# Kernel optimization log

Hardware: AMD Instinct MI355X
Metric: run time of the kernel (lower is better)

The kernel has to match this reference:

```python
import jax, jax.numpy as jnp
import numpy as np
import math

B, S, H = 2, 2048, 2048
NH, NKV, HD = 16, 8, 128          # heads, kv heads, head_dim
GROUPS = NH // NKV                 # 2
FF = 5632
EPS = 1e-6
SCALE = 0.02


def setup_inputs() -> dict:
    key = jax.random.key(0)
    ks = jax.random.split(key, 12)
    def w(k, shape):
        return jax.random.normal(k, shape, dtype=jnp.float32) * SCALE
    # additive causal mask: 0 on/below diagonal, -inf above
    causal = jnp.where(jnp.tril(jnp.ones((S, S), dtype=bool)), 0.0, -jnp.inf)
    attention_mask = causal[None, None].astype(jnp.float32)  # [1,1,S,S]
    return {
        "hidden_states": jax.random.normal(ks[0], (B, S, H), dtype=jnp.float32),
        "attention_mask": attention_mask,
        "q_w": w(ks[1], (NH * HD, H)),      # nn.Linear convention [out, in]
        "k_w": w(ks[2], (NKV * HD, H)),
        "v_w": w(ks[3], (NKV * HD, H)),
        "o_w": w(ks[4], (H, NH * HD)),
        "gate_w": w(ks[5], (FF, H)),
        "up_w": w(ks[6], (FF, H)),
        "down_w": w(ks[7], (H, FF)),
        "ln1_w": jnp.ones((H,), dtype=jnp.float32),
        "ln2_w": jnp.ones((H,), dtype=jnp.float32),
    }


def rmsnorm(x, w):
    var = jnp.mean(jnp.square(x), axis=-1, keepdims=True)
    return x * jax.lax.rsqrt(var + EPS) * w


def attention(x, mask, q_w, k_w, v_w, o_w):
    b, s, _ = x.shape
    q = (x @ q_w.T).reshape(b, s, NH, HD).transpose(0, 2, 1, 3)    # [b,nh,s,hd]
    k = (x @ k_w.T).reshape(b, s, NKV, HD).transpose(0, 2, 1, 3)   # [b,nkv,s,hd]
    v = (x @ v_w.T).reshape(b, s, NKV, HD).transpose(0, 2, 1, 3)
    # GQA: repeat_interleave kv heads to match query heads
    k = jnp.repeat(k, GROUPS, axis=1)
    v = jnp.repeat(v, GROUPS, axis=1)
    scores = jnp.einsum("bhqd,bhkd->bhqk", q, k) / math.sqrt(HD) + mask
    probs = jax.nn.softmax(scores.astype(jnp.float32), axis=-1).astype(q.dtype)
    out = jnp.einsum("bhqk,bhkd->bhqd", probs, v)
    out = out.transpose(0, 2, 1, 3).reshape(b, s, NH * HD)
    return out @ o_w.T


def mlp(x, gate_w, up_w, down_w):
    return (jax.nn.silu(x @ gate_w.T) * (x @ up_w.T)) @ down_w.T


def reference(hidden_states, attention_mask, q_w, k_w, v_w, o_w,
              gate_w, up_w, down_w, ln1_w, ln2_w):
    # pre-norm transformer layer with residuals
    h = hidden_states + attention(rmsnorm(hidden_states, ln1_w), attention_mask,
                                  q_w, k_w, v_w, o_w)
    out = h + mlp(rmsnorm(h, ln2_w), gate_w, up_w, down_w)
    return out
```

## Files before the change

kernel.cpp:

```cpp
#include <hip/hip_runtime.h>
#include <stdint.h>

typedef __bf16 bf16_t;
typedef __bf16 bf16x8 __attribute__((ext_vector_type(8)));
typedef __bf16 bf16x4 __attribute__((ext_vector_type(4)));
typedef float  f32x4  __attribute__((ext_vector_type(4)));

#define MFMA16(a, b, c) __builtin_amdgcn_mfma_f32_16x16x32_bf16((a), (b), (c), 0, 0, 0)

__device__ __forceinline__ void load_lds16(const bf16_t* g, bf16_t* l)
{
    __builtin_amdgcn_global_load_lds(
        (const __attribute__((address_space(1))) uint32_t*)(uintptr_t)g,
        (__attribute__((address_space(3))) uint32_t*)(uint32_t)(uintptr_t)l,
        16, 0, 0);
}

__device__ __forceinline__ void lds_stage2(const bf16_t* __restrict__ Gsrc,
                                           bf16_t* Ldst, int u0,
                                           int tid, int K, int k0)
{
#pragma unroll
    for (int l = 0; l < 2; ++l) {
        int u = u0 + l * 512 + tid;
        int row = u >> 3;
        int col = (((u & 7) ^ (row & 7)) << 3);
        load_lds16(Gsrc + (size_t)row * K + k0 + col, Ldst + u * 8);
    }
}

__global__ __launch_bounds__(256)
void wconv(const float* __restrict__ X, bf16_t* __restrict__ Y, int n)
{
    int i = (blockIdx.x * 256 + threadIdx.x) * 8;
    if (i >= n) return;
    f32x4 a = *(const f32x4*)(X + i);
    f32x4 b = *(const f32x4*)(X + i + 4);
    bf16x8 y;
#pragma unroll
    for (int e = 0; e < 4; ++e) { y[e] = (bf16_t)a[e]; y[e + 4] = (bf16_t)b[e]; }
    *(bf16x8*)(Y + i) = y;
}

__global__ __launch_bounds__(256)
void rmsnorm_f32(const float* __restrict__ X, const float* __restrict__ Wt,
                 bf16_t* __restrict__ Y)
{
    __shared__ float red[4];
    const int tid = threadIdx.x;
    const size_t row = blockIdx.x;
    const float* x = X + row * 2048;

    f32x4 x0 = *(const f32x4*)(x + tid * 8);
    f32x4 x1 = *(const f32x4*)(x + tid * 8 + 4);
    float ss = 0.f;
#pragma unroll
    for (int e = 0; e < 4; ++e) ss += x0[e] * x0[e] + x1[e] * x1[e];
#pragma unroll
    for (int off = 32; off; off >>= 1) ss += __shfl_xor(ss, off, 64);
    if ((tid & 63) == 0) red[tid >> 6] = ss;
    __syncthreads();
    float tot = red[0] + red[1] + red[2] + red[3];
    float scale = rsqrtf(tot * (1.f / 2048.f) + 1e-6f);

    f32x4 w0 = *(const f32x4*)(Wt + tid * 8);
    f32x4 w1 = *(const f32x4*)(Wt + tid * 8 + 4);
    bf16x8 yv;
#pragma unroll
    for (int e = 0; e < 4; ++e) {
        yv[e]     = (bf16_t)(x0[e] * scale * w0[e]);
        yv[e + 4] = (bf16_t)(x1[e] * scale * w1[e]);
    }
    *(bf16x8*)(Y + row * 2048 + tid * 8) = yv;
}

__global__ __launch_bounds__(256)
void rmsnorm_bf16(const bf16_t* __restrict__ X, const float* __restrict__ Wt,
                  bf16_t* __restrict__ Y)
{
    __shared__ float red[4];
    const int tid = threadIdx.x;
    const size_t row = blockIdx.x;

    bf16x8 xv = *(const bf16x8*)(X + row * 2048 + tid * 8);
    float xf[8];
    float ss = 0.f;
#pragma unroll
    for (int e = 0; e < 8; ++e) { xf[e] = (float)xv[e]; ss += xf[e] * xf[e]; }
#pragma unroll
    for (int off = 32; off; off >>= 1) ss += __shfl_xor(ss, off, 64);
    if ((tid & 63) == 0) red[tid >> 6] = ss;
    __syncthreads();
    float tot = red[0] + red[1] + red[2] + red[3];
    float scale = rsqrtf(tot * (1.f / 2048.f) + 1e-6f);

    f32x4 w0 = *(const f32x4*)(Wt + tid * 8);
    f32x4 w1 = *(const f32x4*)(Wt + tid * 8 + 4);
    bf16x8 yv;
#pragma unroll
    for (int e = 0; e < 4; ++e) {
        yv[e]     = (bf16_t)(xf[e] * scale * w0[e]);
        yv[e + 4] = (bf16_t)(xf[e + 4] * scale * w1[e]);
    }
    *(bf16x8*)(Y + row * 2048 + tid * 8) = yv;
}

__global__ __launch_bounds__(512, 2)
void gemm8(const bf16_t* __restrict__ A, const bf16_t* __restrict__ W,
           const float* __restrict__ Rf, const bf16_t* __restrict__ Rb,
           bf16_t* __restrict__ Cb, bf16_t* __restrict__ Cb2,
           float* __restrict__ Cf,
           int M, int N, int K, int nbx, int mode)
{
    __shared__ bf16_t As[2][256 * 64];
    __shared__ bf16_t Ws[2][128 * 64];

    const int tid  = threadIdx.x;
    const int lane = tid & 63, wave = tid >> 6;
    const int quad = lane >> 4, l16 = lane & 15;
    const int wr = wave >> 1, wc = wave & 1;

    const int lid = (int)blockIdx.x;
    const int nwg = (M >> 8) * nbx;
    const int q   = nwg >> 3;
    const int swz = (lid & 7) * q + (lid >> 3);
    const int bxn = swz >> 4;
    const int bym = swz & 15;
    const int m0 = bym * 256, n0 = bxn * 128;

    const bf16_t* Ab = A + (size_t)m0 * K;
    const bf16_t* Wb = W + (size_t)n0 * K;

    const int xsw  = (l16 & 7) << 3;
    const int aoff = (wr * 64 + l16) * 64;
    const int boff = (wc * 64 + l16) * 64;

    f32x4 acc[4][4] = {};

    lds_stage2(Ab, As[0], 0,    tid, K, 0);
    lds_stage2(Ab, As[0], 1024, tid, K, 0);
    lds_stage2(Wb, Ws[0], 0,    tid, K, 0);

    const int NT = K >> 6;
    for (int t = 0; t < NT; ++t) {
        const int b  = t & 1;
        const int kn = (t + 1) << 6;
        const bool pf = (t + 1 < NT);
        bf16_t* An = As[1 - b];
        bf16_t* Wn = Ws[1 - b];

        if (pf) {
            lds_stage2(Ab, An, 0, tid, K, kn);
            asm volatile("s_waitcnt vmcnt(2)" ::: "memory");
        } else {
            asm volatile("s_waitcnt vmcnt(0)" ::: "memory");
        }
        __builtin_amdgcn_s_barrier();

        const bf16_t* Asb = As[b];
        const bf16_t* Wsb = Ws[b];

#pragma unroll
        for (int ks = 0; ks < 2; ++ks) {
            const int kxo = (ks * 32 + quad * 8) ^ xsw;
            bf16x8 af[4], bf_[4];
#pragma unroll
            for (int i = 0; i < 4; ++i)
                af[i] = *(const bf16x8*)(Asb + aoff + i * 1024 + kxo);
#pragma unroll
            for (int j = 0; j < 4; ++j)
                bf_[j] = *(const bf16x8*)(Wsb + boff + j * 1024 + kxo);
            if (pf) {
                if (ks == 0) lds_stage2(Ab, An, 1024, tid, K, kn);
                else         lds_stage2(Wb, Wn, 0,    tid, K, kn);
            }
            __builtin_amdgcn_s_barrier();
            __builtin_amdgcn_s_setprio(1);
#pragma unroll
            for (int i = 0; i < 4; ++i)
#pragma unroll
                for (int j = 0; j < 4; ++j)
                    acc[i][j] = MFMA16(af[i], bf_[j], acc[i][j]);
            __builtin_amdgcn_s_setprio(0);
            __builtin_amdgcn_s_barrier();
        }
    }

    bf16_t* dst5 = (n0 < 1024) ? Cb : Cb2;

#pragma unroll
    for (int i = 0; i < 4; ++i)
#pragma unroll
        for (int j = 0; j < 4; ++j)
#pragma unroll
            for (int r = 0; r < 4; ++r) {
                size_t row = (size_t)(m0 + wr * 64 + i * 16 + quad * 4 + r);
                size_t col = (size_t)(n0 + wc * 64 + j * 16 + l16);
                float v = acc[i][j][r];
                if (mode == 1) v += Rf[row * (size_t)N + col];
                if (mode == 2)
                    Cf[row * (size_t)N + col] = v + (float)Rb[row * (size_t)N + col];
                else if (mode == 5)
                    dst5[row * 1024 + (col & 1023)] = (bf16_t)v;
                else
                    Cb[row * (size_t)N + col] = (bf16_t)v;
            }
}

__global__ __launch_bounds__(512, 2)
void gateup8(const bf16_t* __restrict__ A, const bf16_t* __restrict__ G,
             const bf16_t* __restrict__ U, bf16_t* __restrict__ C,
             int M, int N, int K)
{
    __shared__ bf16_t As[2][256 * 64];
    __shared__ bf16_t Gs[2][128 * 64];
    __shared__ bf16_t Us[2][128 * 64];

    const int tid  = threadIdx.x;
    const int lane = tid & 63;
    const int wave = tid >> 6;
    const int quad = lane >> 4, l16 = lane & 15;
    const int wr = wave >> 2, wc = wave & 3;

    const int lid = (int)blockIdx.x;
    const int nwg = (M >> 8) * (N >> 7);
    const int cpx = nwg >> 3;
    const int swz = (lid & 7) * cpx + (lid >> 3);
    const int bxn = swz >> 4;
    const int bym = swz & 15;
    const int m0 = bym * 256, n0 = bxn * 128;

    const bf16_t* Ab = A + (size_t)m0 * K;
    const bf16_t* Gb = G + (size_t)n0 * K;
    const bf16_t* Ub = U + (size_t)n0 * K;

    const int xsw  = (l16 & 7) << 3;
    const int aoff = (wr * 128 + l16) * 64;
    const int boff = (wc * 32 + l16) * 64;

    f32x4 accg[8][2] = {};
    f32x4 accu[8][2] = {};

    lds_stage2(Ab, As[0], 0,    tid, K, 0);
    lds_stage2(Ab, As[0], 1024, tid, K, 0);
    lds_stage2(Gb, Gs[0], 0,    tid, K, 0);
    lds_stage2(Ub, Us[0], 0,    tid, K, 0);

    const int NT = K >> 6;
    for (int t = 0; t < NT; ++t) {
        const int b  = t & 1;
        const int kn = (t + 1) << 6;
        const bool pf = (t + 1 < NT);
        bf16_t* An = As[1 - b];
        bf16_t* Gn = Gs[1 - b];
        bf16_t* Un = Us[1 - b];

        if (pf) {
            lds_stage2(Ab, An, 0, tid, K, kn);
            asm volatile("s_waitcnt vmcnt(2)" ::: "memory");
        } else {
            asm volatile("s_waitcnt vmcnt(0)" ::: "memory");
        }
        __builtin_amdgcn_s_barrier();

        const bf16_t* Asb = As[b];
        const bf16_t* Gsb = Gs[b];
        const bf16_t* Usb = Us[b];

        bf16x8 af[4], bg[2], bu[2];

        {
            const int kxo = (quad * 8) ^ xsw;
#pragma unroll
            for (int i = 0; i < 4; ++i)
                af[i] = *(const bf16x8*)(Asb + aoff + i * 1024 + kxo);
#pragma unroll
            for (int j = 0; j < 2; ++j) {
                bg[j] = *(const bf16x8*)(Gsb + boff + j * 1024 + kxo);
                bu[j] = *(const bf16x8*)(Usb + boff + j * 1024 + kxo);
            }
        }
        if (pf) lds_stage2(Ab, An, 1024, tid, K, kn);
        __builtin_amdgcn_s_barrier();
        __builtin_amdgcn_s_setprio(1);
#pragma unroll
        for (int i = 0; i < 4; ++i)
#pragma unroll
            for (int j = 0; j < 2; ++j) {
                accg[i][j] = MFMA16(af[i], bg[j], accg[i][j]);
                accu[i][j] = MFMA16(af[i], bu[j], accu[i][j]);
            }
        __builtin_amdgcn_s_setprio(0);
        __builtin_amdgcn_s_barrier();

        {
            const int kxo = (quad * 8) ^ xsw;
#pragma unroll
            for (int i = 0; i < 4; ++i)
                af[i] = *(const bf16x8*)(Asb + aoff + (i + 4) * 1024 + kxo);
        }
        if (pf) lds_stage2(Gb, Gn, 0, tid, K, kn);
        __builtin_amdgcn_s_barrier();
        __builtin_amdgcn_s_setprio(1);
#pragma unroll
        for (int i = 0; i < 4; ++i)
#pragma unroll
            for (int j = 0; j < 2; ++j) {
                accg[i + 4][j] = MFMA16(af[i], bg[j], accg[i + 4][j]);
                accu[i + 4][j] = MFMA16(af[i], bu[j], accu[i + 4][j]);
            }
        __builtin_amdgcn_s_setprio(0);
        __builtin_amdgcn_s_barrier();

        {
            const int kxo = (32 + quad * 8) ^ xsw;
#pragma unroll
            for (int i = 0; i < 4; ++i)
                af[i] = *(const bf16x8*)(Asb + aoff + i * 1024 + kxo);
#pragma unroll
            for (int j = 0; j < 2; ++j) {
                bg[j] = *(const bf16x8*)(Gsb + boff + j * 1024 + kxo);
                bu[j] = *(const bf16x8*)(Usb + boff + j * 1024 + kxo);
            }
        }
        if (pf) lds_stage2(Ub, Un, 0, tid, K, kn);
        __builtin_amdgcn_s_barrier();
        __builtin_amdgcn_s_setprio(1);
#pragma unroll
        for (int i = 0; i < 4; ++i)
#pragma unroll
            for (int j = 0; j < 2; ++j) {
                accg[i][j] = MFMA16(af[i], bg[j], accg[i][j]);
                accu[i][j] = MFMA16(af[i], bu[j], accu[i][j]);
            }
        __builtin_amdgcn_s_setprio(0);
        __builtin_amdgcn_s_barrier();

        {
            const int kxo = (32 + quad * 8) ^ xsw;
#pragma unroll
            for (int i = 0; i < 4; ++i)
                af[i] = *(const bf16x8*)(Asb + aoff + (i + 4) * 1024 + kxo);
        }
        __builtin_amdgcn_s_barrier();
        __builtin_amdgcn_s_setprio(1);
#pragma unroll
        for (int i = 0; i < 4; ++i)
#pragma unroll
            for (int j = 0; j < 2; ++j) {
                accg[i + 4][j] = MFMA16(af[i], bg[j], accg[i + 4][j]);
                accu[i + 4][j] = MFMA16(af[i], bu[j], accu[i + 4][j]);
            }
        __builtin_amdgcn_s_setprio(0);
        __builtin_amdgcn_s_barrier();
    }

#pragma unroll
    for (int i = 0; i < 8; ++i)
#pragma unroll
        for (int j = 0; j < 2; ++j)
#pragma unroll
            for (int r = 0; r < 4; ++r) {
                size_t row = (size_t)(m0 + wr * 128 + i * 16 + quad * 4 + r);
                size_t col = (size_t)(n0 + wc * 32 + j * 16 + l16);
                float g = accg[i][j][r];
                float u = accu[i][j][r];
                float sig = 1.f / (1.f + __expf(fminf(-g, 80.f)));
                C[row * (size_t)N + col] = (bf16_t)(g * sig * u);
            }
}

__global__ __launch_bounds__(256, 2)
void gemm_bt(const bf16_t* __restrict__ A, const float* __restrict__ W,
             const float* __restrict__ Rf, const bf16_t* __restrict__ Rb,
             bf16_t* __restrict__ Cb, float* __restrict__ Cf,
             int M, int N, int K, int mode)
{
    __shared__ bf16_t As[128 * 64];
    __shared__ bf16_t Ws[128 * 64];

    const int tid  = threadIdx.x;
    const int lane = tid & 63, wave = tid >> 6;
    const int quad = lane >> 4, l16 = lane & 15;
    const int m0 = blockIdx.y * 128, n0 = blockIdx.x * 128;
    const int wm = (wave >> 1) * 64, wn = (wave & 1) * 64;

    f32x4 acc[4][4] = {};

    for (int k0 = 0; k0 < K; k0 += 64) {
        bf16x8 ra[4];
        bf16x4 rw[8];
#pragma unroll
        for (int i = 0; i < 4; ++i) {
            int u = i * 256 + tid;
            int r = u >> 3, c = (u & 7) << 3;
            ra[i] = *(const bf16x8*)(A + (size_t)(m0 + r) * K + k0 + c);
        }
#pragma unroll
        for (int i = 0; i < 8; ++i) {
            int u = i * 256 + tid;
            int r = u >> 4, c = (u & 15) << 2;
            f32x4 w4 = *(const f32x4*)(W + (size_t)(n0 + r) * K + k0 + c);
#pragma unroll
            for (int e = 0; e < 4; ++e) rw[i][e] = (bf16_t)w4[e];
        }
        __syncthreads();
#pragma unroll
        for (int i = 0; i < 4; ++i)
            *(bf16x8*)(As + (i * 256 + tid) * 8) = ra[i];
#pragma unroll
        for (int i = 0; i < 8; ++i)
            *(bf16x4*)(Ws + (i * 256 + tid) * 4) = rw[i];
        __syncthreads();

#pragma unroll
        for (int ks = 0; ks < 64; ks += 32) {
            bf16x8 af[4], bfr[4];
#pragma unroll
            for (int i = 0; i < 4; ++i)
                af[i] = *(const bf16x8*)(As + (wm + i * 16 + l16) * 64 + ks + quad * 8);
#pragma unroll
            for (int j = 0; j < 4; ++j)
                bfr[j] = *(const bf16x8*)(Ws + (wn + j * 16 + l16) * 64 + ks + quad * 8);
#pragma unroll
            for (int i = 0; i < 4; ++i)
#pragma unroll
                for (int j = 0; j < 4; ++j)
                    acc[i][j] = MFMA16(af[i], bfr[j], acc[i][j]);
        }
    }

#pragma unroll
    for (int i = 0; i < 4; ++i)
#pragma unroll
        for (int j = 0; j < 4; ++j)
#pragma unroll
            for (int r = 0; r < 4; ++r) {
                size_t row = (size_t)(m0 + wm + i * 16 + quad * 4 + r);
                size_t col = (size_t)(n0 + wn + j * 16 + l16);
                float v = acc[i][j][r];
                if (mode == 1) v += Rf[row * (size_t)N + col];
                if (mode == 2)
                    Cf[row * (size_t)N + col] = v + (float)Rb[row * (size_t)N + col];
                else
                    Cb[row * (size_t)N + col] = (bf16_t)v;
            }
}

__global__ __launch_bounds__(256, 2)
void gemm_gateup(const bf16_t* __restrict__ A, const float* __restrict__ G,
                 const float* __restrict__ U, bf16_t* __restrict__ C,
                 int M, int N, int K)
{
    __shared__ bf16_t As[128 * 64];
    __shared__ bf16_t Gs[128 * 64];
    __shared__ bf16_t Us[128 * 64];

    const int tid  = threadIdx.x;
    const int lane = tid & 63, wave = tid >> 6;
    const int quad = lane >> 4, l16 = lane & 15;
    const int m0 = blockIdx.y * 128, n0 = blockIdx.x * 128;
    const int wm = (wave >> 1) * 64, wn = (wave & 1) * 64;

    f32x4 accg[4][4] = {};
    f32x4 accu[4][4] = {};

    for (int k0 = 0; k0 < K; k0 += 64) {
        bf16x8 ra[4];
        bf16x4 rg[8], ru[8];
#pragma unroll
        for (int i = 0; i < 4; ++i) {
            int u = i * 256 + tid;
            int r = u >> 3, c = (u & 7) << 3;
            ra[i] = *(const bf16x8*)(A + (size_t)(m0 + r) * K + k0 + c);
        }
#pragma unroll
        for (int i = 0; i < 8; ++i) {
            int u = i * 256 + tid;
            int r = u >> 4, c = (u & 15) << 2;
            f32x4 g4 = *(const f32x4*)(G + (size_t)(n0 + r) * K + k0 + c);
            f32x4 u4 = *(const f32x4*)(U + (size_t)(n0 + r) * K + k0 + c);
#pragma unroll
            for (int e = 0; e < 4; ++e) { rg[i][e] = (bf16_t)g4[e]; ru[i][e] = (bf16_t)u4[e]; }
        }
        __syncthreads();
#pragma unroll
        for (int i = 0; i < 4; ++i)
            *(bf16x8*)(As + (i * 256 + tid) * 8) = ra[i];
#pragma unroll
        for (int i = 0; i < 8; ++i) {
            *(bf16x4*)(Gs + (i * 256 + tid) * 4) = rg[i];
            *(bf16x4*)(Us + (i * 256 + tid) * 4) = ru[i];
        }
        __syncthreads();

#pragma unroll
        for (int ks = 0; ks < 64; ks += 32) {
            bf16x8 af[4], bg[4], bu[4];
#pragma unroll
            for (int i = 0; i < 4; ++i)
                af[i] = *(const bf16x8*)(As + (wm + i * 16 + l16) * 64 + ks + quad * 8);
#pragma unroll
            for (int j = 0; j < 4; ++j) {
                bg[j] = *(const bf16x8*)(Gs + (wn + j * 16 + l16) * 64 + ks + quad * 8);
                bu[j] = *(const bf16x8*)(Us + (wn + j * 16 + l16) * 64 + ks + quad * 8);
            }
#pragma unroll
            for (int i = 0; i < 4; ++i)
#pragma unroll
                for (int j = 0; j < 4; ++j) {
                    accg[i][j] = MFMA16(af[i], bg[j], accg[i][j]);
                    accu[i][j] = MFMA16(af[i], bu[j], accu[i][j]);
                }
        }
    }

#pragma unroll
    for (int i = 0; i < 4; ++i)
#pragma unroll
        for (int j = 0; j < 4; ++j)
#pragma unroll
            for (int r = 0; r < 4; ++r) {
                size_t row = (size_t)(m0 + wm + i * 16 + quad * 4 + r);
                size_t col = (size_t)(n0 + wn + j * 16 + l16);
                float g = accg[i][j][r];
                float u = accu[i][j][r];
                float sig = 1.f / (1.f + __expf(fminf(-g, 80.f)));
                C[row * (size_t)N + col] = (bf16_t)(g * sig * u);
            }
}

__global__ __launch_bounds__(256, 2)
void attn_fwd(const bf16_t* __restrict__ Q, const bf16_t* __restrict__ Kg,
              const bf16_t* __restrict__ Vg, bf16_t* __restrict__ O, int kvs)
{
    __shared__ bf16_t Ks[2][64 * 128];
    __shared__ bf16_t Vt[2][128 * 64];
    __shared__ bf16_t Pl[4][16 * 72];

    const int tid  = threadIdx.x;
    const int lane = tid & 63, wave = tid >> 6;
    const int quad = lane >> 4, l16 = lane & 15;
    const int bh = blockIdx.y, b = bh >> 4, h = bh & 15;

    const bf16_t* Qh = Q  + (size_t)b * 2048 * 2048 + (size_t)h * 128;
    const bf16_t* Kh = Kg + (size_t)b * 2048 * kvs + (size_t)(h >> 1) * 128;
    const bf16_t* Vh = Vg + (size_t)b * 2048 * kvs + (size_t)(h >> 1) * 128;

    const float scale = 0.08838834764831845f;

    const int krow = tid >> 4;
    const int kcol = (tid & 15) << 3;
    const int vd   = tid & 127;
    const int vkb  = tid >> 7;

#pragma unroll 1
    for (int pass = 0; pass < 2; ++pass) {
        const int qt = pass ? (31 - (int)blockIdx.x) : (int)blockIdx.x;
        const int q0 = qt * 64;

        bf16x8 aq[4];
#pragma unroll
        for (int ks = 0; ks < 4; ++ks)
            aq[ks] = *(const bf16x8*)(Qh + (size_t)(q0 + wave * 16 + l16) * 2048 + ks * 32 + quad * 8);

        float m_r[4] = { -30000.f, -30000.f, -30000.f, -30000.f };
        float l_r[4] = { 0.f, 0.f, 0.f, 0.f };
        f32x4 acc_o[8] = {};

        const int ntiles = qt + 1;

        bf16x8 rk[4], rv[4];
#pragma unroll
        for (int i = 0; i < 4; ++i)
            rk[i] = *(const bf16x8*)(Kh + (size_t)(i * 16 + krow) * kvs + kcol);
#pragma unroll
        for (int it = 0; it < 4; ++it)
#pragma unroll
            for (int j = 0; j < 8; ++j)
                rv[it][j] = Vh[(size_t)((vkb + 2 * it) * 8 + j) * kvs + vd];
#pragma unroll
        for (int i = 0; i < 4; ++i) {
            int row = i * 16 + krow;
            *(bf16x8*)(&Ks[0][row * 128 + (kcol ^ ((row & 7) << 3))]) = rk[i];
        }
#pragma unroll
        for (int it = 0; it < 4; ++it) {
            int kb = vkb + 2 * it;
            *(bf16x8*)(&Vt[0][vd * 64 + ((kb ^ (vd & 7)) << 3)]) = rv[it];
        }
        __syncthreads();

        for (int t = 0; t < ntiles; ++t) {
            const int bb = t & 1;
            const bool pf = (t + 1 < ntiles);
            const int kv0 = t * 64;
            const int kvn = kv0 + 64;

            if (pf) {
#pragma unroll
                for (int i = 0; i < 4; ++i)
                    rk[i] = *(const bf16x8*)(Kh + (size_t)(kvn + i * 16 + krow) * kvs + kcol);
#pragma unroll
                for (int it = 0; it < 4; ++it)
#pragma unroll
                    for (int j = 0; j < 8; ++j)
                        rv[it][j] = Vh[(size_t)(kvn + (vkb + 2 * it) * 8 + j) * kvs + vd];
            }

            f32x4 accs[4] = {};
#pragma unroll
            for (int ks = 0; ks < 4; ++ks)
#pragma unroll
                for (int j = 0; j < 4; ++j) {
                    const int row = j * 16 + l16;
                    bf16x8 bk = *(const bf16x8*)(&Ks[bb][row * 128 + ((ks * 32 + quad * 8) ^ ((row & 7) << 3))]);
                    accs[j] = MFMA16(aq[ks], bk, accs[j]);
                }

#pragma unroll
            for (int r = 0; r < 4; ++r) {
                const int qrow = q0 + wave * 16 + quad * 4 + r;
                float s[4];
                float mx = -30000.f;
#pragma unroll
                for (int j = 0; j < 4; ++j) {
                    s[j] = accs[j][r] * scale;
                    if (kv0 + j * 16 + l16 > qrow) s[j] = -30000.f;
                    mx = fmaxf(mx, s[j]);
                }
                mx = fmaxf(mx, __shfl_xor(mx, 1, 64));
                mx = fmaxf(mx, __shfl_xor(mx, 2, 64));
                mx = fmaxf(mx, __shfl_xor(mx, 4, 64));
                mx = fmaxf(mx, __shfl_xor(mx, 8, 64));
                float mnew  = fmaxf(m_r[r], mx);
                float alpha = __expf(fmaxf(m_r[r] - mnew, -80.f));
                float rs = 0.f;
#pragma unroll
                for (int j = 0; j < 4; ++j) {
                    float p = __expf(fmaxf(s[j] - mnew, -80.f));
                    rs += p;
                    Pl[wave][(quad * 4 + r) * 72 + j * 16 + l16] = (bf16_t)p;
                }
                rs += __shfl_xor(rs, 1, 64);
                rs += __shfl_xor(rs, 2, 64);
                rs += __shfl_xor(rs, 4, 64);
                rs += __shfl_xor(rs, 8, 64);
                l_r[r] = l_r[r] * alpha + rs;
                m_r[r] = mnew;
#pragma unroll
                for (int nt = 0; nt < 8; ++nt) acc_o[nt][r] *= alpha;
            }

#pragma unroll
            for (int ks2 = 0; ks2 < 2; ++ks2) {
                bf16x8 ap = *(const bf16x8*)(&Pl[wave][l16 * 72 + ks2 * 32 + quad * 8]);
                const int kb_r = ks2 * 4 + quad;
#pragma unroll
                for (int nt = 0; nt < 8; ++nt) {
                    const int d = nt * 16 + l16;
                    bf16x8 bv = *(const bf16x8*)(&Vt[bb][d * 64 + ((kb_r ^ (d & 7)) << 3)]);
                    acc_o[nt] = MFMA16(ap, bv, acc_o[nt]);
                }
            }

            if (pf) {
#pragma unroll
                for (int i = 0; i < 4; ++i) {
                    int row = i * 16 + krow;
                    *(bf16x8*)(&Ks[1 - bb][row * 128 + (kcol ^ ((row & 7) << 3))]) = rk[i];
                }
#pragma unroll
                for (int it = 0; it < 4; ++it) {
                    int kb = vkb + 2 * it;
                    *(bf16x8*)(&Vt[1 - bb][vd * 64 + ((kb ^ (vd & 7)) << 3)]) = rv[it];
                }
            }
            __syncthreads();
        }

#pragma unroll
        for (int r = 0; r < 4; ++r) {
            float inv = 1.f / fmaxf(l_r[r], 1e-30f);
            size_t orow = (size_t)b * 2048 + q0 + wave * 16 + quad * 4 + r;
#pragma unroll
            for (int nt = 0; nt < 8; ++nt)
                O[orow * 2048 + h * 128 + nt * 16 + l16] = (bf16_t)(acc_o[nt][r] * inv);
        }
    }
}

extern "C" void kernel_launch(void* const* d_in, const int* in_sizes, int n_in,
                              void* d_out, int out_size, void* d_ws, size_t ws_size,
                              hipStream_t stream)
{
    const float* x   = (const float*)d_in[0];
    const float* qw  = (const float*)d_in[2];
    const float* kw  = (const float*)d_in[3];
    const float* vw  = (const float*)d_in[4];
    const float* ow  = (const float*)d_in[5];
    const float* gw  = (const float*)d_in[6];
    const float* uw  = (const float*)d_in[7];
    const float* dw  = (const float*)d_in[8];
    const float* ln1 = (const float*)d_in[9];
    const float* ln2 = (const float*)d_in[10];
    float*  out = (float*)d_out;
    bf16_t* ws  = (bf16_t*)d_ws;

    dim3 blk(256);
    const size_t NEED = 87031808ull * 2;

    if (ws_size >= NEED) {
        bf16_t* wq = ws;
        bf16_t* wk = ws + 4194304;
        bf16_t* wv = ws + 6291456;
        bf16_t* wo = ws + 8388608;
        bf16_t* wg = ws + 12582912;
        bf16_t* wu = ws + 24117248;
        bf16_t* wd = ws + 35651584;
        bf16_t* h1 = ws + 47185920;
        bf16_t* qb = ws + 55574528;
        bf16_t* kb = ws + 63963136;
        bf16_t* vb = ws + 68157440;
        bf16_t* ab = (bf16_t*)d_out;
        bf16_t* hb = qb;
        bf16_t* gb = kb;

        wconv<<<2048, blk, 0, stream>>>(qw, wq, 4194304);
        wconv<<<1024, blk, 0, stream>>>(kw, wk, 2097152);
        wconv<<<1024, blk, 0, stream>>>(vw, wv, 2097152);
        wconv<<<2048, blk, 0, stream>>>(ow, wo, 4194304);
        wconv<<<5632, blk, 0, stream>>>(gw, wg, 11534336);
        wconv<<<5632, blk, 0, stream>>>(uw, wu, 11534336);
        wconv<<<5632, blk, 0, stream>>>(dw, wd, 11534336);

        rmsnorm_f32<<<4096, blk, 0, stream>>>(x, ln1, h1);
        gemm8<<<256, dim3(512), 0, stream>>>(h1, wq, nullptr, nullptr, qb, nullptr, nullptr, 4096, 2048, 2048, 16, 0);
        gemm8<<<256, dim3(512), 0, stream>>>(h1, wk, nullptr, nullptr, kb, vb, nullptr, 4096, 2048, 2048, 16, 5);
        attn_fwd<<<dim3(16, 32), blk, 0, stream>>>(qb, kb, vb, ab, 1024);
        gemm8<<<256, dim3(512), 0, stream>>>(ab, wo, x, nullptr, hb, nullptr, nullptr, 4096, 2048, 2048, 16, 1);
        rmsnorm_bf16<<<4096, blk, 0, stream>>>(hb, ln2, h1);
        gateup8<<<704, dim3(512), 0, stream>>>(h1, wg, wu, gb, 4096, 5632, 2048);
        gemm8<<<256, dim3(512), 0, stream>>>(gb, wd, nullptr, hb, nullptr, nullptr, out, 4096, 2048, 5632, 16, 2);
    } else {
        const size_t ME = 1ull << 20;
        bf16_t* h1 = ws;
        bf16_t* qb = ws + 8  * ME;
        bf16_t* kb = ws + 16 * ME;
        bf16_t* vb = ws + 20 * ME;
        bf16_t* ab = (bf16_t*)d_out;
        bf16_t* hb = ws + 8  * ME;
        bf16_t* gb = ws + 16 * ME;

        rmsnorm_f32<<<4096, blk, 0, stream>>>(x, ln1, h1);
        gemm_bt<<<dim3(16, 32), blk, 0, stream>>>(h1, qw, nullptr, nullptr, qb, nullptr, 4096, 2048, 2048, 0);
        gemm_bt<<<dim3( 8, 32), blk, 0, stream>>>(h1, kw, nullptr, nullptr, kb, nullptr, 4096, 1024, 2048, 0);
        gemm_bt<<<dim3( 8, 32), blk, 0, stream>>>(h1, vw, nullptr, nullptr, vb, nullptr, 4096, 1024, 2048, 0);
        attn_fwd<<<dim3(16, 32), blk, 0, stream>>>(qb, kb, vb, ab, 1024);
        gemm_bt<<<dim3(16, 32), blk, 0, stream>>>(ab, ow, x, nullptr, hb, nullptr, 4096, 2048, 2048, 1);
        rmsnorm_bf16<<<4096, blk, 0, stream>>>(hb, ln2, h1);
        gemm_gateup<<<dim3(44, 32), blk, 0, stream>>>(h1, gw, uw, gb, 4096, 5632, 2048);
        gemm_bt<<<dim3(16, 32), blk, 0, stream>>>(gb, dw, nullptr, hb, nullptr, out, 4096, 2048, 5632, 2);
    }
}
```

Measured before the change: 818.8 us.

## Fuse QKV projection into one 256x256-tile GEMM and merge weight conversions

Replaces the separate Q and KV projection GEMMs with one gemm_qkv kernel that uses 256x256 tiles over the concatenated Q/K/V weight rows, and scatters outputs into the Q, K and V buffers. The seven weight-conversion launches become a single wconv_all launch. In attention, the causal mask test now runs only on the diagonal tile, and s_setprio is raised around the MFMA blocks. The goal is fewer launches and one larger, better-filled projection GEMM, at the cost of a one-block-per-CU launch bound with more accumulator registers.

```diff
diff --git a/kernel.cpp b/kernel.cpp
--- a/kernel.cpp
+++ b/kernel.cpp
@@ -30,16 +30,28 @@
 }
 
 __global__ __launch_bounds__(256)
-void wconv(const float* __restrict__ X, bf16_t* __restrict__ Y, int n)
-{
-    int i = (blockIdx.x * 256 + threadIdx.x) * 8;
-    if (i >= n) return;
-    f32x4 a = *(const f32x4*)(X + i);
-    f32x4 b = *(const f32x4*)(X + i + 4);
+void wconv_all(const float* __restrict__ qw, const float* __restrict__ kw,
+               const float* __restrict__ vw, const float* __restrict__ ow,
+               const float* __restrict__ gw, const float* __restrict__ uw,
+               const float* __restrict__ dw, bf16_t* __restrict__ ws)
+{
+    const int blk = blockIdx.x;
+    const float* src; bf16_t* dst; int off;
+    if      (blk <  2048) { src = qw; dst = ws;            off = blk;         }
+    else if (blk <  3072) { src = kw; dst = ws +  4194304; off = blk -  2048; }
+    else if (blk <  4096) { src = vw; dst = ws +  6291456; off = blk -  3072; }
+    else if (blk <  6144) { src = ow; dst = ws +  8388608; off = blk -  4096; }
+    else if (blk < 11776) { src = gw; dst = ws + 12582912; off = blk -  6144; }
+    else if (blk < 17408) { src = uw; dst = ws + 24117248; off = blk - 11776; }
+    else                  { src = dw; dst = ws + 35651584; off = blk - 17408; }
+
+    int i = (off * 256 + threadIdx.x) * 8;
+    f32x4 a = *(const f32x4*)(src + i);
+    f32x4 b = *(const f32x4*)(src + i + 4);
     bf16x8 y;
 #pragma unroll
     for (int e = 0; e < 4; ++e) { y[e] = (bf16_t)a[e]; y[e + 4] = (bf16_t)b[e]; }
-    *(bf16x8*)(Y + i) = y;
+    *(bf16x8*)(dst + i) = y;
 }
 
 __global__ __launch_bounds__(256)
@@ -105,11 +117,151 @@
     *(bf16x8*)(Y + row * 2048 + tid * 8) = yv;
 }
 
+__global__ __launch_bounds__(512, 1)
+void gemm_qkv(const bf16_t* __restrict__ A, const bf16_t* __restrict__ W,
+              bf16_t* __restrict__ Qb, bf16_t* __restrict__ Kb,
+              bf16_t* __restrict__ Vb, int K)
+{
+    __shared__ bf16_t As[2][256 * 64];
+    __shared__ bf16_t Ws[2][256 * 64];
+
+    const int tid  = threadIdx.x;
+    const int lane = tid & 63, wave = tid >> 6;
+    const int quad = lane >> 4, l16 = lane & 15;
+    const int wr = wave >> 2, wc = wave & 3;
+
+    const int lid = (int)blockIdx.x;
+    const int swz = (lid & 7) * 32 + (lid >> 3);
+    const int bym = swz & 15, bxn = swz >> 4;
+    const int m0 = bym * 256, n0 = bxn * 256;
+
+    const bf16_t* Ab = A + (size_t)m0 * K;
+    const bf16_t* Wb = W + (size_t)n0 * K;
+
+    const int xsw  = (l16 & 7) << 3;
+    const int aoff = (wr * 128 + l16) * 64;
+    const int boff = (wc * 64 + l16) * 64;
+
+    f32x4 acc[8][4] = {};
+
+    lds_stage2(Ab, As[0], 0,    tid, K, 0);
+    lds_stage2(Ab, As[0], 1024, tid, K, 0);
+    lds_stage2(Wb, Ws[0], 0,    tid, K, 0);
+    lds_stage2(Wb, Ws[0], 1024, tid, K, 0);
+
+    const int NT = K >> 6;
+    for (int t = 0; t < NT; ++t) {
+        const int b  = t & 1;
+        const int kn = (t + 1) << 6;
+        const bool pf = (t + 1 < NT);
+        bf16_t* An = As[1 - b];
+        bf16_t* Wn = Ws[1 - b];
+
+        if (pf) {
+            lds_stage2(Ab, An, 0, tid, K, kn);
+            asm volatile("s_waitcnt vmcnt(2)" ::: "memory");
+        } else {
+            asm volatile("s_waitcnt vmcnt(0)" ::: "memory");
+        }
+        __builtin_amdgcn_s_barrier();
+
+        const bf16_t* Asb = As[b];
+        const bf16_t* Wsb = Ws[b];
+        bf16x8 af[4], bb[4];
+
+        {
+            const int kxo = (quad * 8) ^ xsw;
+#pragma unroll
+            for (int i = 0; i < 4; ++i)
+                af[i] = *(const bf16x8*)(Asb + aoff + i * 1024 + kxo);
+#pragma unroll
+            for (int j = 0; j < 4; ++j)
+                bb[j] = *(const bf16x8*)(Wsb + boff + j * 1024 + kxo);
+        }
+        if (pf) lds_stage2(Ab, An, 1024, tid, K, kn);
+        __builtin_amdgcn_s_barrier();
+        __builtin_amdgcn_s_setprio(1);
+#pragma unroll
+        for (int i = 0; i < 4; ++i)
+#pragma unroll
+            for (int j = 0; j < 4; ++j)
+                acc[i][j] = MFMA16(af[i], bb[j], acc[i][j]);
+        __builtin_amdgcn_s_setprio(0);
+        __builtin_amdgcn_s_barrier();
+
+        {
+            const int kxo = (quad * 8) ^ xsw;
+#pragma unroll
+            for (int i = 0; i < 4; ++i)
+                af[i] = *(const bf16x8*)(Asb + aoff + (i + 4) * 1024 + kxo);
+        }
+        if (pf) lds_stage2(Wb, Wn, 0, tid, K, kn);
+        __builtin_amdgcn_s_barrier();
+        __builtin_amdgcn_s_setprio(1);
+#pragma unroll
+        for (int i = 0; i < 4; ++i)
+#pragma unroll
+            for (int j = 0; j < 4; ++j)
+                acc[i + 4][j] = MFMA16(af[i], bb[j], acc[i + 4][j]);
+        __builtin_amdgcn_s_setprio(0);
+        __builtin_amdgcn_s_barrier();
+
+        {
+            const int kxo = (32 + quad * 8) ^ xsw;
+#pragma unroll
+            for (int i = 0; i < 4; ++i)
+                af[i] = *(const bf16x8*)(Asb + aoff + i * 1024 + kxo);
+#pragma unroll
+            for (int j = 0; j < 4; ++j)
+                bb[j] = *(const bf16x8*)(Wsb + boff + j * 1024 + kxo);
+        }
+        if (pf) lds_stage2(Wb, Wn, 1024, tid, K, kn);
+        __builtin_amdgcn_s_barrier();
+        __builtin_amdgcn_s_setprio(1);
+#pragma unroll
+        for (int i = 0; i < 4; ++i)
+#pragma unroll
+            for (int j = 0; j < 4; ++j)
+                acc[i][j] = MFMA16(af[i], bb[j], acc[i][j]);
+        __builtin_amdgcn_s_setprio(0);
+        __builtin_amdgcn_s_barrier();
+
+        {
+            const int kxo = (32 + quad * 8) ^ xsw;
+#pragma unroll
+            for (int i = 0; i < 4; ++i)
+                af[i] = *(const bf16x8*)(Asb + aoff + (i + 4) * 1024 + kxo);
+        }
+        __builtin_amdgcn_s_barrier();
+        __builtin_amdgcn_s_setprio(1);
+#pragma unroll
+        for (int i = 0; i < 4; ++i)
+#pragma unroll
+            for (int j = 0; j < 4; ++j)
+                acc[i + 4][j] = MFMA16(af[i], bb[j], acc[i + 4][j]);
+        __builtin_amdgcn_s_setprio(0);
+        __builtin_amdgcn_s_barrier();
+    }
+
+#pragma unroll
+    for (int i = 0; i < 8; ++i)
+#pragma unroll
+        for (int j = 0; j < 4; ++j)
+#pragma unroll
+            for (int r = 0; r < 4; ++r) {
+                size_t row = (size_t)(m0 + wr * 128 + i * 16 + quad * 4 + r);
+                int    col = n0 + wc * 64 + j * 16 + l16;
+                bf16_t v = (bf16_t)acc[i][j][r];
+                if (col < 2048)      Qb[row * 2048 + col] = v;
+                else if (col < 3072) Kb[row * 1024 + (col - 2048)] = v;
+                else                 Vb[row * 1024 + (col - 3072)] = v;
+            }
+}
+
 __global__ __launch_bounds__(512, 2)
 void gemm8(const bf16_t* __restrict__ A, const bf16_t* __restrict__ W,
            const float* __restrict__ Rf, const bf16_t* __restrict__ Rb,
-           bf16_t* __restrict__ Cb, bf16_t* __restrict__ Cb2,
-           float* __restrict__ Cf,
+           bf16_t* __restrict__ Cb, float* __restrict__ Cf,
            int M, int N, int K, int nbx, int mode)
 {
     __shared__ bf16_t As[2][256 * 64];
@@ -186,8 +338,6 @@
         }
     }
 
-    bf16_t* dst5 = (n0 < 1024) ? Cb : Cb2;
-
 #pragma unroll
     for (int i = 0; i < 4; ++i)
 #pragma unroll
@@ -200,8 +350,6 @@
                 if (mode == 1) v += Rf[row * (size_t)N + col];
                 if (mode == 2)
                     Cf[row * (size_t)N + col] = v + (float)Rb[row * (size_t)N + col];
-                else if (mode == 5)
-                    dst5[row * 1024 + (col & 1023)] = (bf16_t)v;
                 else
                     Cb[row * (size_t)N + col] = (bf16_t)v;
             }
@@ -594,6 +742,7 @@
         for (int t = 0; t < ntiles; ++t) {
             const int bb = t & 1;
             const bool pf = (t + 1 < ntiles);
+            const bool diag = (t == qt);
             const int kv0 = t * 64;
             const int kvn = kv0 + 64;
 
@@ -609,6 +758,7 @@
             }
 
             f32x4 accs[4] = {};
+            __builtin_amdgcn_s_setprio(1);
 #pragma unroll
             for (int ks = 0; ks < 4; ++ks)
 #pragma unroll
@@ -617,18 +767,20 @@
                     bf16x8 bk = *(const bf16x8*)(&Ks[bb][row * 128 + ((ks * 32 + quad * 8) ^ ((row & 7) << 3))]);
                     accs[j] = MFMA16(aq[ks], bk, accs[j]);
                 }
+            __builtin_amdgcn_s_setprio(0);
 
 #pragma unroll
             for (int r = 0; r < 4; ++r) {
                 const int qrow = q0 + wave * 16 + quad * 4 + r;
                 float s[4];
-                float mx = -30000.f;
-#pragma unroll
-                for (int j = 0; j < 4; ++j) {
-                    s[j] = accs[j][r] * scale;
-                    if (kv0 + j * 16 + l16 > qrow) s[j] = -30000.f;
-                    mx = fmaxf(mx, s[j]);
+#pragma unroll
+                for (int j = 0; j < 4; ++j) s[j] = accs[j][r] * scale;
+                if (diag) {
+#pragma unroll
+                    for (int j = 0; j < 4; ++j)
+                        if (kv0 + j * 16 + l16 > qrow) s[j] = -30000.f;
                 }
+                float mx = fmaxf(fmaxf(s[0], s[1]), fmaxf(s[2], s[3]));
                 mx = fmaxf(mx, __shfl_xor(mx, 1, 64));
                 mx = fmaxf(mx, __shfl_xor(mx, 2, 64));
                 mx = fmaxf(mx, __shfl_xor(mx, 4, 64));
@@ -652,6 +804,7 @@
                 for (int nt = 0; nt < 8; ++nt) acc_o[nt][r] *= alpha;
             }
 
+            __builtin_amdgcn_s_setprio(1);
 #pragma unroll
             for (int ks2 = 0; ks2 < 2; ++ks2) {
                 bf16x8 ap = *(const bf16x8*)(&Pl[wave][l16 * 72 + ks2 * 32 + quad * 8]);
@@ -663,6 +816,7 @@
                     acc_o[nt] = MFMA16(ap, bv, acc_o[nt]);
                 }
             }
+            __builtin_amdgcn_s_setprio(0);
 
             if (pf) {
 #pragma unroll
@@ -712,8 +866,6 @@
 
     if (ws_size >= NEED) {
         bf16_t* wq = ws;
-        bf16_t* wk = ws + 4194304;
-        bf16_t* wv = ws + 6291456;
         bf16_t* wo = ws + 8388608;
         bf16_t* wg = ws + 12582912;
         bf16_t* wu = ws + 24117248;
@@ -726,22 +878,14 @@
         bf16_t* hb = qb;
         bf16_t* gb = kb;
 
-        wconv<<<2048, blk, 0, stream>>>(qw, wq, 4194304);
-        wconv<<<1024, blk, 0, stream>>>(kw, wk, 2097152);
-        wconv<<<1024, blk, 0, stream>>>(vw, wv, 2097152);
-        wconv<<<2048, blk, 0, stream>>>(ow, wo, 4194304);
-        wconv<<<5632, blk, 0, stream>>>(gw, wg, 11534336);
-        wconv<<<5632, blk, 0, stream>>>(uw, wu, 11534336);
-        wconv<<<5632, blk, 0, stream>>>(dw, wd, 11534336);
-
+        wconv_all<<<23040, blk, 0, stream>>>(qw, kw, vw, ow, gw, uw, dw, ws);
         rmsnorm_f32<<<4096, blk, 0, stream>>>(x, ln1, h1);
-        gemm8<<<256, dim3(512), 0, stream>>>(h1, wq, nullptr, nullptr, qb, nullptr, nullptr, 4096, 2048, 2048, 16, 0);
-        gemm8<<<256, dim3(512), 0, stream>>>(h1, wk, nullptr, nullptr, kb, vb, nullptr, 4096, 2048, 2048, 16, 5);
+        gemm_qkv<<<256, dim3(512), 0, stream>>>(h1, wq, qb, kb, vb, 2048);
         attn_fwd<<<dim3(16, 32), blk, 0, stream>>>(qb, kb, vb, ab, 1024);
-        gemm8<<<256, dim3(512), 0, stream>>>(ab, wo, x, nullptr, hb, nullptr, nullptr, 4096, 2048, 2048, 16, 1);
+        gemm8<<<256, dim3(512), 0, stream>>>(ab, wo, x, nullptr, hb, nullptr, 4096, 2048, 2048, 16, 1);
         rmsnorm_bf16<<<4096, blk, 0, stream>>>(hb, ln2, h1);
         gateup8<<<704, dim3(512), 0, stream>>>(h1, wg, wu, gb, 4096, 5632, 2048);
-        gemm8<<<256, dim3(512), 0, stream>>>(gb, wd, nullptr, hb, nullptr, nullptr, out, 4096, 2048, 5632, 16, 2);
+        gemm8<<<256, dim3(512), 0, stream>>>(gb, wd, nullptr, hb, nullptr, out, 4096, 2048, 5632, 16, 2);
     } else {
         const size_t ME = 1ull << 20;
         bf16_t* h1 = ws;
```

Result: faster. 787.4 us (-3.8%).
